# Kernel optimization log

Measured on AMD Instinct MI355X. Metric: run time of the kernel, lower is better.

Reference implementation:

```python
import jax, jax.numpy as jnp
import numpy as np

EPS = 1e-5
D, H, W = 2, 4, 4          # fixed patch grid from the rearrange string
P = 8                       # p1*p2*p3 = 2*2*2 tokens per patch


def setup_inputs() -> dict:
    key = jax.random.key(0)
    k1, k2, k3, k4, k5 = jax.random.split(key, 5)
    c, heads = 128, 8
    B = 16 * D * H * W  # 512 patches (b=16)
    emb = jax.random.normal(k1, (B, P, c), dtype=jnp.float32)
    s = 1.0 / np.sqrt(c)
    Wq = jax.random.normal(k2, (c, c * heads), dtype=jnp.float32) * s
    Wk = jax.random.normal(k3, (c, c * heads), dtype=jnp.float32) * s
    Wv = jax.random.normal(k4, (c, c * heads), dtype=jnp.float32) * s
    Wout = jax.random.normal(k5, (c * heads, c), dtype=jnp.float32) * (1.0 / np.sqrt(c * heads))
    return {"emb": emb, "Wq": Wq, "Wk": Wk, "Wv": Wv, "Wout": Wout}


def reference(emb, Wq, Wk, Wv, Wout):
    B, n, c = emb.shape            # B = b*32, n = 8
    heads = Wq.shape[1] // c
    b = B // (D * H * W)

    q = emb @ Wq                   # (B, 8, c*heads)
    k = emb @ Wk
    v = emb @ Wv

    # '(p) (c heads)' -> heads c p  /  heads p c
    mh_q = q.reshape(B, P, c, heads).transpose(0, 3, 2, 1)   # (B, heads, c, P)
    mh_k = k.reshape(B, P, c, heads).transpose(0, 3, 1, 2)   # (B, heads, P, c)
    mh_v = v.reshape(B, P, c, heads).transpose(0, 3, 2, 1)   # (B, heads, c, P)

    attn = jnp.einsum('bhcp,bhpe->bhce', mh_q, mh_k)         # (B, heads, c, c) channel scores

    # InstanceNorm2d(num_heads): normalize each (patch, head) c x c map (biased var)
    mu = attn.mean(axis=(2, 3), keepdims=True)
    var = attn.var(axis=(2, 3), keepdims=True)
    attn = (attn - mu) * jax.lax.rsqrt(var + EPS)

    attn = jax.nn.softmax(attn, axis=3)
    ctx = jnp.einsum('bhce,bhep->bhcp', attn, mh_v)          # (B, heads, c, P)

    # '(b d h w) heads c (p1 p2 p3) -> b (d p1 h p2 w p3) (c heads)'
    ctx = ctx.reshape(b, D, H, W, heads, c, 2, 2, 2)
    ctx = ctx.transpose(0, 1, 6, 2, 7, 3, 8, 5, 4)           # b d p1 h p2 w p3 c heads
    ctx = ctx.reshape(b, D * 2 * H * 2 * W * 2, c * heads)   # (b, 256, c*heads)

    return ctx @ Wout                                        # (b, 256, c)
```

## Files before the change

kernel.cpp:

```cpp
#include <hip/hip_runtime.h>
#include <hip/hip_bf16.h>
#include <math.h>


typedef short bfrag __attribute__((ext_vector_type(8)));
typedef float f32x4 __attribute__((ext_vector_type(4)));

static __device__ __forceinline__ short f2bf(float x) {
    __hip_bfloat16 h = __float2bfloat16(x);
    return __builtin_bit_cast(short, h);
}
static __device__ __forceinline__ bfrag bzero() {
    bfrag z;
    #pragma unroll
    for (int j = 0; j < 8; ++j) z[j] = 0;
    return z;
}

__global__ __launch_bounds__(256) void convertW(
    const float* __restrict__ Wq, const float* __restrict__ Wk,
    const float* __restrict__ Wv, const float* __restrict__ Wout,
    short* __restrict__ Wp, short* __restrict__ Wout_pt)
{
    __shared__ short lt[128 * 33];
    const int b = blockIdx.x, t = threadIdx.x;
    if (b < 96) {
        const int x = b >> 5, h = (b >> 2) & 7, k0 = (b & 3) * 32;
        const float* W = (x == 0) ? Wq : (x == 1) ? Wk : Wv;
        #pragma unroll 4
        for (int rr = 0; rr < 16; ++rr) {
            const int k = rr * 2 + (t >> 7);
            const int i = t & 127;
            lt[k * 129 + i] = f2bf(W[(k0 + k) * 1024 + i * 8 + h]);
        }
        __syncthreads();
        short* dst = Wp + (x * 8 + h) * 16384;
        #pragma unroll
        for (int pp = 0; pp < 4; ++pp) {
            const int i  = pp * 32 + (t >> 3);
            const int kk = (t & 7) * 4;
            short4 v;
            v.x = lt[(kk + 0) * 129 + i]; v.y = lt[(kk + 1) * 129 + i];
            v.z = lt[(kk + 2) * 129 + i]; v.w = lt[(kk + 3) * 129 + i];
            *(short4*)&dst[i * 128 + k0 + kk] = v;
        }
    } else {
        const int b2 = b - 96, h = b2 >> 2, c0 = (b2 & 3) * 32;
        #pragma unroll 4
        for (int rr = 0; rr < 16; ++rr) {
            const int i = rr * 8 + (t >> 5);
            const int c = t & 31;
            lt[i * 33 + c] = f2bf(Wout[(i * 8 + h) * 128 + c0 + c]);
        }
        __syncthreads();
        short* dst = Wout_pt + h * 16384;
        #pragma unroll
        for (int pp = 0; pp < 4; ++pp) {
            const int c  = pp * 8 + (t >> 5);
            const int i0 = (t & 31) * 4;
            short4 v;
            v.x = lt[(i0 + 0) * 33 + c]; v.y = lt[(i0 + 1) * 33 + c];
            v.z = lt[(i0 + 2) * 33 + c]; v.w = lt[(i0 + 3) * 33 + c];
            *(short4*)&dst[(c0 + c) * 128 + i0] = v;
        }
    }
}

#define QT   0
#define KT   4096
#define QN   8192
#define KN   12288
#define VS   16384
#define CTXo 16384

__global__ __launch_bounds__(256, 4) void attn4(
    const float* __restrict__ emb,
    const short* __restrict__ Wp,
    const short* __restrict__ Wout_pt,
    float* __restrict__ part)
{
    __shared__ short lds[20480];
    const int bid = blockIdx.x;
    const int pg  = bid >> 3;
    const int h   = bid & 7;
    const int t   = threadIdx.x;
    const int w    = t >> 6;
    const int lane = t & 63;
    const int m16  = lane & 15;
    const int quad = lane >> 4;
    const int q8   = quad * 8;

    {
        bfrag a[2][4];
        #pragma unroll
        for (int tm = 0; tm < 2; ++tm)
            #pragma unroll
            for (int ks = 0; ks < 4; ++ks) {
                const float* er = emb + (size_t)(pg*32 + tm*16 + m16) * 128 + ks*32 + q8;
                const float4 x0 = *(const float4*)er;
                const float4 x1 = *(const float4*)(er + 4);
                bfrag f;
                f[0]=f2bf(x0.x); f[1]=f2bf(x0.y); f[2]=f2bf(x0.z); f[3]=f2bf(x0.w);
                f[4]=f2bf(x1.x); f[5]=f2bf(x1.y); f[6]=f2bf(x1.z); f[7]=f2bf(x1.w);
                a[tm][ks] = f;
            }

        #pragma unroll
        for (int tt = 0; tt < 6; ++tt) {
            const int nt = w * 6 + tt;
            const int x  = nt >> 3;
            const int i0 = (nt & 7) * 16;
            const short* Wb = Wp + ((x*8 + h)*128 + i0 + m16) * 128;
            bfrag bb[4];
            #pragma unroll
            for (int ks = 0; ks < 4; ++ks)
                bb[ks] = *(const bfrag*)&Wb[ks*32 + q8];
            f32x4 c0 = {0.f,0.f,0.f,0.f}, c1 = {0.f,0.f,0.f,0.f};
            #pragma unroll
            for (int ks = 0; ks < 4; ++ks) {
                c0 = __builtin_amdgcn_mfma_f32_16x16x32_bf16(a[0][ks], bb[ks], c0, 0,0,0);
                c1 = __builtin_amdgcn_mfma_f32_16x16x32_bf16(a[1][ks], bb[ks], c1, 0,0,0);
            }
            #pragma unroll
            for (int tm = 0; tm < 2; ++tm) {
                const f32x4 cc = tm ? c1 : c0;
                const int mrow0 = tm*16 + quad*4;
                const int pl = mrow0 >> 3;
                const int p0 = mrow0 & 7;
                const int col = i0 + m16;
                if (x == 0) {
                    short4 v;
                    v.x = f2bf(cc[0]); v.y = f2bf(cc[1]);
                    v.z = f2bf(cc[2]); v.w = f2bf(cc[3]);
                    *(short4*)&lds[QT + pl*1024 + col*8 + p0] = v;
                    #pragma unroll
                    for (int r = 0; r < 4; ++r)
                        lds[QN + pl*1024 + (p0 + r)*128 + col] = f2bf(cc[r]);
                } else if (x == 1) {
                    short4 v;
                    v.x = f2bf(cc[0]); v.y = f2bf(cc[1]);
                    v.z = f2bf(cc[2]); v.w = f2bf(cc[3]);
                    *(short4*)&lds[KT + pl*1024 + col*8 + p0] = v;
                    #pragma unroll
                    for (int r = 0; r < 4; ++r)
                        lds[KN + pl*1024 + (p0 + r)*128 + col] = f2bf(cc[r]);
                } else {
                    #pragma unroll
                    for (int r = 0; r < 4; ++r)
                        lds[VS + pl*1024 + (p0 + r)*128 + col] = f2bf(cc[r]);
                }
            }
        }
    }
    __syncthreads();

    float rs2, nbias;
    {
        bfrag gq[4], gk[4], gs[4], ones;
        #pragma unroll
        for (int j = 0; j < 8; ++j) ones[j] = (short)0x3F80;
        #pragma unroll
        for (int ks = 0; ks < 4; ++ks) {
            gq[ks] = (m16 < 8) ? *(const bfrag*)&lds[QN + w*1024 + m16*128 + ks*32 + q8] : bzero();
            gk[ks] = (m16 < 8) ? *(const bfrag*)&lds[KN + w*1024 + m16*128 + ks*32 + q8] : bzero();
            gs[ks] = (m16 < 8) ? *(const bfrag*)&lds[QN + w*1024 + m16*128 + ks*32 + q8]
                               : *(const bfrag*)&lds[KN + w*1024 + (m16 - 8)*128 + ks*32 + q8];
        }
        f32x4 cg = {0.f,0.f,0.f,0.f}, ch = {0.f,0.f,0.f,0.f}, cs = {0.f,0.f,0.f,0.f};
        #pragma unroll
        for (int ks = 0; ks < 4; ++ks) {
            cg = __builtin_amdgcn_mfma_f32_16x16x32_bf16(gq[ks], gq[ks], cg, 0,0,0);
            ch = __builtin_amdgcn_mfma_f32_16x16x32_bf16(gk[ks], gk[ks], ch, 0,0,0);
            cs = __builtin_amdgcn_mfma_f32_16x16x32_bf16(gs[ks], ones,  cs, 0,0,0);
        }
        float gh = 0.f, sp = 0.f;
        #pragma unroll
        for (int r = 0; r < 4; ++r) {
            gh = fmaf(cg[r], ch[r], gh);
            sp = fmaf(cs[r], __shfl_xor(cs[r], 32), sp);
        }
        sp += __shfl_xor(sp, 16);
        #pragma unroll
        for (int off = 1; off <= 32; off <<= 1)
            gh += __shfl_xor(gh, off);
        const float mean = sp * (1.f / 16384.f);
        const float var  = gh * (1.f / 16384.f) - mean * mean;
        rs2   = rsqrtf(var + 1e-5f) * 1.44269504f;
        nbias = -mean * rs2;
    }

    bfrag bs[8], av[4];
    #pragma unroll
    for (int nt = 0; nt < 8; ++nt)
        bs[nt] = (quad == 0) ? *(const bfrag*)&lds[KT + w*1024 + (nt*16 + m16)*8] : bzero();
    #pragma unroll
    for (int ks = 0; ks < 4; ++ks) {
        if (m16 < 8)
            av[ks] = *(const bfrag*)&lds[VS + w*1024 + m16*128 + ks*32 + q8];
        else if (m16 == 8) {
            bfrag o;
            #pragma unroll
            for (int j = 0; j < 8; ++j) o[j] = (short)0x3F80;
            av[ks] = o;
        } else
            av[ks] = bzero();
    }
    __syncthreads();

    short* ps = &lds[QN + w*2048];
    f32x4 c[8];
    {
        const bfrag am = (quad == 0) ? *(const bfrag*)&lds[QT + w*1024 + m16*8] : bzero();
        #pragma unroll
        for (int nt = 0; nt < 8; ++nt) {
            f32x4 z = {0.f,0.f,0.f,0.f};
            c[nt] = __builtin_amdgcn_mfma_f32_16x16x32_bf16(am, bs[nt], z, 0,0,0);
        }
    }
    #pragma unroll 1
    for (int mb = 0; mb < 8; ++mb) {
        #pragma unroll
        for (int nt = 0; nt < 8; ++nt)
            #pragma unroll
            for (int r = 0; r < 4; ++r) {
                const int row = quad*4 + r;
                ps[row*128 + ((nt ^ (row & 7)) << 4) + m16] =
                    f2bf(exp2f(fmaf(c[nt][r], rs2, nbias)));
            }
        if (mb < 7) {
            const bfrag am = (quad == 0)
                ? *(const bfrag*)&lds[QT + w*1024 + ((mb+1)*16 + m16)*8] : bzero();
            #pragma unroll
            for (int nt = 0; nt < 8; ++nt) {
                f32x4 z = {0.f,0.f,0.f,0.f};
                c[nt] = __builtin_amdgcn_mfma_f32_16x16x32_bf16(am, bs[nt], z, 0,0,0);
            }
        }
        f32x4 cc = {0.f,0.f,0.f,0.f};
        #pragma unroll
        for (int ks = 0; ks < 4; ++ks) {
            const bfrag bp = *(const bfrag*)
                &ps[m16*128 + (((2*ks + (quad >> 1)) ^ (m16 & 7)) << 4) + (quad & 1)*8];
            cc = __builtin_amdgcn_mfma_f32_16x16x32_bf16(av[ks], bp, cc, 0,0,0);
        }
        const float s  = __shfl(cc[0], 32 + m16);
        const float is = 1.0f / s;
        if (quad < 2) {
            #pragma unroll
            for (int r = 0; r < 4; ++r)
                lds[CTXo + w*1024 + (quad*4 + r)*128 + mb*16 + m16] = f2bf(cc[r] * is);
        }
    }

    bfrag ac[4];
    #pragma unroll
    for (int ks = 0; ks < 4; ++ks)
        ac[ks] = (m16 < 8) ? *(const bfrag*)&lds[CTXo + w*1024 + m16*128 + ks*32 + q8]
                           : bzero();
    const short* Wo = Wout_pt + h * 16384;
    float* pb = part + (size_t)h * 524288 + (size_t)(pg*4 + w) * 8 * 128;
    #pragma unroll 1
    for (int nt = 0; nt < 8; ++nt) {
        f32x4 cc = {0.f,0.f,0.f,0.f};
        #pragma unroll
        for (int ks = 0; ks < 4; ++ks) {
            const bfrag wb = *(const bfrag*)&Wo[(nt*16 + m16)*128 + ks*32 + q8];
            cc = __builtin_amdgcn_mfma_f32_16x16x32_bf16(ac[ks], wb, cc, 0,0,0);
        }
        if (quad < 2) {
            #pragma unroll
            for (int r = 0; r < 4; ++r)
                pb[(quad*4 + r)*128 + nt*16 + m16] = cc[r];
        }
    }
}

__global__ __launch_bounds__(256) void reduce8(
    const float* __restrict__ part, float* __restrict__ out)
{
    const int f = blockIdx.x * 256 + threadIdx.x;
    const int rowf = f >> 5, c4 = f & 31;
    const int pat = rowf >> 3, p = rowf & 7;
    const int bb = pat >> 5, rem = pat & 31;
    const int dd = rem >> 4, hh = (rem >> 2) & 3, ww = rem & 3;
    const int p1 = p >> 2, p2 = (p >> 1) & 1, p3 = p & 1;
    const int orow = bb*256 + ((((dd*2 + p1)*4 + hh)*2 + p2)*4 + ww)*2 + p3;
    const f32x4* p4 = (const f32x4*)part;
    f32x4 s = p4[rowf*32 + c4];
    #pragma unroll
    for (int h = 1; h < 8; ++h)
        s += p4[h*131072 + rowf*32 + c4];
    ((f32x4*)out)[orow*32 + c4] = s;
}

extern "C" void kernel_launch(void* const* d_in, const int* in_sizes, int n_in,
                              void* d_out, int out_size, void* d_ws, size_t ws_size,
                              hipStream_t stream) {
    const float* emb  = (const float*)d_in[0];
    const float* Wq   = (const float*)d_in[1];
    const float* Wk   = (const float*)d_in[2];
    const float* Wv   = (const float*)d_in[3];
    const float* Wout = (const float*)d_in[4];
    float* out = (float*)d_out;

    float* part    = (float*)d_ws;
    short* Wp      = (short*)((char*)d_ws + 16777216);
    short* Wout_pt = Wp + 393216;

    convertW<<<128, 256, 0, stream>>>(Wq, Wk, Wv, Wout, Wp, Wout_pt);
    attn4<<<1024, 256, 0, stream>>>(emb, Wp, Wout_pt, part);
    reduce8<<<512, 256, 0, stream>>>(part, out);
}
```

Baseline: 117.2 us.

## Compute instance-norm stats from score tiles directly, shrink LDS for higher occupancy

Removes the separate QN/KN row-major copies and the Gram-matrix MFMA trick used to get the instance-norm mean and variance. Instead it runs an extra pass over all score tiles, accumulating sum and sum of squares in registers. This frees LDS (20480 to 16384 shorts), so launch bounds can be raised to five blocks per CU. It also swizzles the V and P layouts, reuses the last computed tile to start the softmax loop, and uses the raw exp2 builtin. The trade-off is recomputing the QK^T MFMAs once more per block in exchange for fewer LDS writes and higher occupancy.

```diff
diff --git a/kernel.cpp b/kernel.cpp
--- a/kernel.cpp
+++ b/kernel.cpp
@@ -68,18 +68,16 @@
 
 #define QT   0
 #define KT   4096
-#define QN   8192
-#define KN   12288
-#define VS   16384
-#define CTXo 16384
-
-__global__ __launch_bounds__(256, 4) void attn4(
+#define VS   8192
+#define CTXo 12288
+
+__global__ __launch_bounds__(256, 5) void attn4(
     const float* __restrict__ emb,
     const short* __restrict__ Wp,
     const short* __restrict__ Wout_pt,
     float* __restrict__ part)
 {
-    __shared__ short lds[20480];
+    __shared__ short lds[16384];
     const int bid = blockIdx.x;
     const int pg  = bid >> 3;
     const int h   = bid & 7;
@@ -133,71 +131,69 @@
                     v.x = f2bf(cc[0]); v.y = f2bf(cc[1]);
                     v.z = f2bf(cc[2]); v.w = f2bf(cc[3]);
                     *(short4*)&lds[QT + pl*1024 + col*8 + p0] = v;
-                    #pragma unroll
-                    for (int r = 0; r < 4; ++r)
-                        lds[QN + pl*1024 + (p0 + r)*128 + col] = f2bf(cc[r]);
                 } else if (x == 1) {
                     short4 v;
                     v.x = f2bf(cc[0]); v.y = f2bf(cc[1]);
                     v.z = f2bf(cc[2]); v.w = f2bf(cc[3]);
                     *(short4*)&lds[KT + pl*1024 + col*8 + p0] = v;
+                } else {
+                    const int g = (((nt & 7) ^ (((pl & 1) << 1) | (p0 >> 2))) << 4);
                     #pragma unroll
                     for (int r = 0; r < 4; ++r)
-                        lds[KN + pl*1024 + (p0 + r)*128 + col] = f2bf(cc[r]);
-                } else {
-                    #pragma unroll
-                    for (int r = 0; r < 4; ++r)
-                        lds[VS + pl*1024 + (p0 + r)*128 + col] = f2bf(cc[r]);
+                        lds[VS + pl*1024 + (p0 + r)*128 + g + m16] = f2bf(cc[r]);
                 }
             }
         }
     }
     __syncthreads();
 
-    float rs2, nbias;
-    {
-        bfrag gq[4], gk[4], gs[4], ones;
-        #pragma unroll
-        for (int j = 0; j < 8; ++j) ones[j] = (short)0x3F80;
-        #pragma unroll
-        for (int ks = 0; ks < 4; ++ks) {
-            gq[ks] = (m16 < 8) ? *(const bfrag*)&lds[QN + w*1024 + m16*128 + ks*32 + q8] : bzero();
-            gk[ks] = (m16 < 8) ? *(const bfrag*)&lds[KN + w*1024 + m16*128 + ks*32 + q8] : bzero();
-            gs[ks] = (m16 < 8) ? *(const bfrag*)&lds[QN + w*1024 + m16*128 + ks*32 + q8]
-                               : *(const bfrag*)&lds[KN + w*1024 + (m16 - 8)*128 + ks*32 + q8];
-        }
-        f32x4 cg = {0.f,0.f,0.f,0.f}, ch = {0.f,0.f,0.f,0.f}, cs = {0.f,0.f,0.f,0.f};
-        #pragma unroll
-        for (int ks = 0; ks < 4; ++ks) {
-            cg = __builtin_amdgcn_mfma_f32_16x16x32_bf16(gq[ks], gq[ks], cg, 0,0,0);
-            ch = __builtin_amdgcn_mfma_f32_16x16x32_bf16(gk[ks], gk[ks], ch, 0,0,0);
-            cs = __builtin_amdgcn_mfma_f32_16x16x32_bf16(gs[ks], ones,  cs, 0,0,0);
-        }
-        float gh = 0.f, sp = 0.f;
-        #pragma unroll
-        for (int r = 0; r < 4; ++r) {
-            gh = fmaf(cg[r], ch[r], gh);
-            sp = fmaf(cs[r], __shfl_xor(cs[r], 32), sp);
-        }
-        sp += __shfl_xor(sp, 16);
-        #pragma unroll
-        for (int off = 1; off <= 32; off <<= 1)
-            gh += __shfl_xor(gh, off);
-        const float mean = sp * (1.f / 16384.f);
-        const float var  = gh * (1.f / 16384.f) - mean * mean;
-        rs2   = rsqrtf(var + 1e-5f) * 1.44269504f;
-        nbias = -mean * rs2;
-    }
-
-    bfrag bs[8], av[4];
+    bfrag bs[8];
     #pragma unroll
     for (int nt = 0; nt < 8; ++nt)
         bs[nt] = (quad == 0) ? *(const bfrag*)&lds[KT + w*1024 + (nt*16 + m16)*8] : bzero();
+
+    f32x4 c[8];
+    float ssum = 0.f, ssq = 0.f;
+    {
+        bfrag am = (quad == 0) ? *(const bfrag*)&lds[QT + w*1024 + m16*8] : bzero();
+        #pragma unroll 1
+        for (int mb = 0; mb < 8; ++mb) {
+            bfrag amn = am;
+            if (mb < 7)
+                amn = (quad == 0)
+                    ? *(const bfrag*)&lds[QT + w*1024 + ((mb+1)*16 + m16)*8] : bzero();
+            #pragma unroll
+            for (int nt = 0; nt < 8; ++nt) {
+                f32x4 z = {0.f,0.f,0.f,0.f};
+                c[nt] = __builtin_amdgcn_mfma_f32_16x16x32_bf16(am, bs[nt], z, 0,0,0);
+            }
+            #pragma unroll
+            for (int nt = 0; nt < 8; ++nt)
+                #pragma unroll
+                for (int r = 0; r < 4; ++r) {
+                    ssum += c[nt][r];
+                    ssq   = fmaf(c[nt][r], c[nt][r], ssq);
+                }
+            am = amn;
+        }
+    }
+    #pragma unroll
+    for (int off = 1; off <= 32; off <<= 1) {
+        ssum += __shfl_xor(ssum, off);
+        ssq  += __shfl_xor(ssq,  off);
+    }
+    const float mean  = ssum * (1.f / 16384.f);
+    const float var   = ssq  * (1.f / 16384.f) - mean * mean;
+    const float rs2   = rsqrtf(var + 1e-5f) * 1.44269504f;
+    const float nbias = -mean * rs2;
+
+    bfrag av[4];
     #pragma unroll
     for (int ks = 0; ks < 4; ++ks) {
-        if (m16 < 8)
-            av[ks] = *(const bfrag*)&lds[VS + w*1024 + m16*128 + ks*32 + q8];
-        else if (m16 == 8) {
+        if (m16 < 8) {
+            const int g = (((2*ks + (quad >> 1)) ^ (((w & 1) << 1) | (m16 >> 2))) << 4);
+            av[ks] = *(const bfrag*)&lds[VS + w*1024 + m16*128 + g + (quad & 1)*8];
+        } else if (m16 == 8) {
             bfrag o;
             #pragma unroll
             for (int j = 0; j < 8; ++j) o[j] = (short)0x3F80;
@@ -207,40 +203,32 @@
     }
     __syncthreads();
 
-    short* ps = &lds[QN + w*2048];
-    f32x4 c[8];
-    {
-        const bfrag am = (quad == 0) ? *(const bfrag*)&lds[QT + w*1024 + m16*8] : bzero();
-        #pragma unroll
-        for (int nt = 0; nt < 8; ++nt) {
-            f32x4 z = {0.f,0.f,0.f,0.f};
-            c[nt] = __builtin_amdgcn_mfma_f32_16x16x32_bf16(am, bs[nt], z, 0,0,0);
-        }
-    }
+    short* ps = &lds[KT + w*2048];
     #pragma unroll 1
-    for (int mb = 0; mb < 8; ++mb) {
+    for (int it = 0; it < 8; ++it) {
+        const int mb = (it + 7) & 7;
         #pragma unroll
         for (int nt = 0; nt < 8; ++nt)
             #pragma unroll
             for (int r = 0; r < 4; ++r) {
                 const int row = quad*4 + r;
-                ps[row*128 + ((nt ^ (row & 7)) << 4) + m16] =
-                    f2bf(exp2f(fmaf(c[nt][r], rs2, nbias)));
-            }
-        if (mb < 7) {
-            const bfrag am = (quad == 0)
-                ? *(const bfrag*)&lds[QT + w*1024 + ((mb+1)*16 + m16)*8] : bzero();
+                ps[row*128 + ((nt ^ quad) << 4) + m16] =
+                    f2bf(__builtin_amdgcn_exp2f(fmaf(c[nt][r], rs2, nbias)));
+            }
+        if (it < 7) {
+            const bfrag am2 = (quad == 0)
+                ? *(const bfrag*)&lds[QT + w*1024 + (it*16 + m16)*8] : bzero();
             #pragma unroll
             for (int nt = 0; nt < 8; ++nt) {
                 f32x4 z = {0.f,0.f,0.f,0.f};
-                c[nt] = __builtin_amdgcn_mfma_f32_16x16x32_bf16(am, bs[nt], z, 0,0,0);
+                c[nt] = __builtin_amdgcn_mfma_f32_16x16x32_bf16(am2, bs[nt], z, 0,0,0);
             }
         }
         f32x4 cc = {0.f,0.f,0.f,0.f};
         #pragma unroll
         for (int ks = 0; ks < 4; ++ks) {
             const bfrag bp = *(const bfrag*)
-                &ps[m16*128 + (((2*ks + (quad >> 1)) ^ (m16 & 7)) << 4) + (quad & 1)*8];
+                &ps[m16*128 + (((2*ks + (quad >> 1)) ^ (m16 >> 2)) << 4) + (quad & 1)*8];
             cc = __builtin_amdgcn_mfma_f32_16x16x32_bf16(av[ks], bp, cc, 0,0,0);
         }
         const float s  = __shfl(cc[0], 32 + m16);
```

Result: slower. 120.1 us (+2.5%).

## Fuse head reduction into attention via atomicAdd and swizzle V/P LDS layouts

Applied to the files above, without the earlier changes.

Removes the separate reduce8 kernel and the 16MB partial buffer: each attention block atomically adds its per-head output projection directly into the permuted output rows, and convertW zeroes the output first. It also changes the XOR swizzle on the V and softmax-probability LDS tiles to cut bank conflicts, and uses the raw hardware exp2 builtin. The cost is float atomic contention across 8 heads per output element and a nondeterministic summation order.

```diff
diff --git a/kernel.cpp b/kernel.cpp
--- a/kernel.cpp
+++ b/kernel.cpp
@@ -20,10 +20,20 @@
 __global__ __launch_bounds__(256) void convertW(
     const float* __restrict__ Wq, const float* __restrict__ Wk,
     const float* __restrict__ Wv, const float* __restrict__ Wout,
-    short* __restrict__ Wp, short* __restrict__ Wout_pt)
+    short* __restrict__ Wp, short* __restrict__ Wout_pt,
+    float* __restrict__ out)
 {
     __shared__ short lt[128 * 33];
     const int b = blockIdx.x, t = threadIdx.x;
+
+    {
+        float4* o4 = (float4*)out;
+        const int zb = b * 1024 + t;
+        #pragma unroll
+        for (int k = 0; k < 4; ++k)
+            o4[zb + k * 256] = make_float4(0.f, 0.f, 0.f, 0.f);
+    }
+
     if (b < 96) {
         const int x = b >> 5, h = (b >> 2) & 7, k0 = (b & 3) * 32;
         const float* W = (x == 0) ? Wq : (x == 1) ? Wk : Wv;
@@ -77,7 +87,7 @@
     const float* __restrict__ emb,
     const short* __restrict__ Wp,
     const short* __restrict__ Wout_pt,
-    float* __restrict__ part)
+    float* __restrict__ out)
 {
     __shared__ short lds[20480];
     const int bid = blockIdx.x;
@@ -145,9 +155,10 @@
                     for (int r = 0; r < 4; ++r)
                         lds[KN + pl*1024 + (p0 + r)*128 + col] = f2bf(cc[r]);
                 } else {
+                    const int g = (((nt & 7) ^ (((pl & 1) << 1) | (p0 >> 2))) << 4);
                     #pragma unroll
                     for (int r = 0; r < 4; ++r)
-                        lds[VS + pl*1024 + (p0 + r)*128 + col] = f2bf(cc[r]);
+                        lds[VS + pl*1024 + (p0 + r)*128 + g + m16] = f2bf(cc[r]);
                 }
             }
         }
@@ -195,9 +206,10 @@
         bs[nt] = (quad == 0) ? *(const bfrag*)&lds[KT + w*1024 + (nt*16 + m16)*8] : bzero();
     #pragma unroll
     for (int ks = 0; ks < 4; ++ks) {
-        if (m16 < 8)
-            av[ks] = *(const bfrag*)&lds[VS + w*1024 + m16*128 + ks*32 + q8];
-        else if (m16 == 8) {
+        if (m16 < 8) {
+            const int g = (((2*ks + (quad >> 1)) ^ (((w & 1) << 1) | (m16 >> 2))) << 4);
+            av[ks] = *(const bfrag*)&lds[VS + w*1024 + m16*128 + g + (quad & 1)*8];
+        } else if (m16 == 8) {
             bfrag o;
             #pragma unroll
             for (int j = 0; j < 8; ++j) o[j] = (short)0x3F80;
@@ -224,8 +236,8 @@
             #pragma unroll
             for (int r = 0; r < 4; ++r) {
                 const int row = quad*4 + r;
-                ps[row*128 + ((nt ^ (row & 7)) << 4) + m16] =
-                    f2bf(exp2f(fmaf(c[nt][r], rs2, nbias)));
+                ps[row*128 + ((nt ^ quad) << 4) + m16] =
+                    f2bf(__builtin_amdgcn_exp2f(fmaf(c[nt][r], rs2, nbias)));
             }
         if (mb < 7) {
             const bfrag am = (quad == 0)
@@ -240,7 +252,7 @@
         #pragma unroll
         for (int ks = 0; ks < 4; ++ks) {
             const bfrag bp = *(const bfrag*)
-                &ps[m16*128 + (((2*ks + (quad >> 1)) ^ (m16 & 7)) << 4) + (quad & 1)*8];
+                &ps[m16*128 + (((2*ks + (quad >> 1)) ^ (m16 >> 2)) << 4) + (quad & 1)*8];
             cc = __builtin_amdgcn_mfma_f32_16x16x32_bf16(av[ks], bp, cc, 0,0,0);
         }
         const float s  = __shfl(cc[0], 32 + m16);
@@ -258,7 +270,9 @@
         ac[ks] = (m16 < 8) ? *(const bfrag*)&lds[CTXo + w*1024 + m16*128 + ks*32 + q8]
                            : bzero();
     const short* Wo = Wout_pt + h * 16384;
-    float* pb = part + (size_t)h * 524288 + (size_t)(pg*4 + w) * 8 * 128;
+    const int pat = pg*4 + w;
+    const int bb = pat >> 5, rem = pat & 31;
+    const int dd = rem >> 4, hh2 = (rem >> 2) & 3, ww2 = rem & 3;
     #pragma unroll 1
     for (int nt = 0; nt < 8; ++nt) {
         f32x4 cc = {0.f,0.f,0.f,0.f};
@@ -269,28 +283,13 @@
         }
         if (quad < 2) {
             #pragma unroll
-            for (int r = 0; r < 4; ++r)
-                pb[(quad*4 + r)*128 + nt*16 + m16] = cc[r];
-        }
-    }
-}
-
-__global__ __launch_bounds__(256) void reduce8(
-    const float* __restrict__ part, float* __restrict__ out)
-{
-    const int f = blockIdx.x * 256 + threadIdx.x;
-    const int rowf = f >> 5, c4 = f & 31;
-    const int pat = rowf >> 3, p = rowf & 7;
-    const int bb = pat >> 5, rem = pat & 31;
-    const int dd = rem >> 4, hh = (rem >> 2) & 3, ww = rem & 3;
-    const int p1 = p >> 2, p2 = (p >> 1) & 1, p3 = p & 1;
-    const int orow = bb*256 + ((((dd*2 + p1)*4 + hh)*2 + p2)*4 + ww)*2 + p3;
-    const f32x4* p4 = (const f32x4*)part;
-    f32x4 s = p4[rowf*32 + c4];
-    #pragma unroll
-    for (int h = 1; h < 8; ++h)
-        s += p4[h*131072 + rowf*32 + c4];
-    ((f32x4*)out)[orow*32 + c4] = s;
+            for (int r = 0; r < 4; ++r) {
+                const int orow = bb*256
+                    + ((((dd*2 + quad)*4 + hh2)*2 + (r >> 1))*4 + ww2)*2 + (r & 1);
+                atomicAdd(&out[(size_t)orow*128 + nt*16 + m16], cc[r]);
+            }
+        }
+    }
 }
 
 extern "C" void kernel_launch(void* const* d_in, const int* in_sizes, int n_in,
@@ -303,11 +302,9 @@
     const float* Wout = (const float*)d_in[4];
     float* out = (float*)d_out;
 
-    float* part    = (float*)d_ws;
-    short* Wp      = (short*)((char*)d_ws + 16777216);
+    short* Wp      = (short*)d_ws;
     short* Wout_pt = Wp + 393216;
 
-    convertW<<<128, 256, 0, stream>>>(Wq, Wk, Wv, Wout, Wp, Wout_pt);
-    attn4<<<1024, 256, 0, stream>>>(emb, Wp, Wout_pt, part);
-    reduce8<<<512, 256, 0, stream>>>(part, out);
-}
+    convertW<<<128, 256, 0, stream>>>(Wq, Wk, Wv, Wout, Wp, Wout_pt, out);
+    attn4<<<1024, 256, 0, stream>>>(emb, Wp, Wout_pt, out);
+}
```

Result: faster. 109.6 us (-6.5%).
